# Optimization experiments

Measured on AMD Instinct MI355X. Metric: run time of the kernel, lower is better.

## Reference

```python
import jax, jax.numpy as jnp
import numpy as np

SPATIAL_SHAPES = [(128, 128), (64, 64), (32, 32), (16, 16)]  # (H_l, W_l) per level
NUM_HEADS = 8
NUM_LEVELS = 4
NUM_POINTS = 4
EMBED_DIM = 256
HEAD_DIM = EMBED_DIM // NUM_HEADS
LEN_V = sum(h * w for h, w in SPATIAL_SHAPES)  # 21760
BS, LQ = 8, 900


def setup_inputs() -> dict:
    key = jax.random.key(0)
    ks = jax.random.split(key, 12)
    s = 0.05
    return {
        'query': jax.random.normal(ks[0], (BS, LQ, EMBED_DIM), jnp.float32),
        'reference_points': jax.random.uniform(ks[1], (BS, LQ, NUM_LEVELS, 2), jnp.float32),
        'value': jax.random.normal(ks[2], (BS, LEN_V, EMBED_DIM), jnp.float32),
        'w_value': jax.random.normal(ks[3], (EMBED_DIM, EMBED_DIM), jnp.float32) * s,
        'b_value': jnp.zeros((EMBED_DIM,), jnp.float32),
        'w_off': jax.random.normal(ks[4], (EMBED_DIM, NUM_HEADS * NUM_LEVELS * NUM_POINTS * 2), jnp.float32) * s,
        'b_off': jax.random.normal(ks[5], (NUM_HEADS * NUM_LEVELS * NUM_POINTS * 2,), jnp.float32),
        'w_attn': jax.random.normal(ks[6], (EMBED_DIM, NUM_HEADS * NUM_LEVELS * NUM_POINTS), jnp.float32) * s,
        'b_attn': jnp.zeros((NUM_HEADS * NUM_LEVELS * NUM_POINTS,), jnp.float32),
        'w_out': jax.random.normal(ks[7], (EMBED_DIM, EMBED_DIM), jnp.float32) * s,
        'b_out': jnp.zeros((EMBED_DIM,), jnp.float32),
    }


def _bilinear_sample(val, locx, locy, H, W):
    # val: [bs, nh, H*W, hd]; locx/locy: [bs, nh, N] normalized in [0,1]
    # grid_sample semantics: align_corners=False, zero padding.
    px = locx * W - 0.5
    py = locy * H - 0.5
    x0 = jnp.floor(px)
    y0 = jnp.floor(py)
    dx = px - x0
    dy = py - y0
    x0i = x0.astype(jnp.int32)
    y0i = y0.astype(jnp.int32)
    out = jnp.zeros(val.shape[:2] + (locx.shape[-1], val.shape[-1]), val.dtype)
    corners = [
        (x0i, y0i, (1 - dx) * (1 - dy)),
        (x0i + 1, y0i, dx * (1 - dy)),
        (x0i, y0i + 1, (1 - dx) * dy),
        (x0i + 1, y0i + 1, dx * dy),
    ]
    for xi, yi, w in corners:
        valid = ((xi >= 0) & (xi < W) & (yi >= 0) & (yi < H)).astype(val.dtype)
        idx = jnp.clip(yi, 0, H - 1) * W + jnp.clip(xi, 0, W - 1)
        g = jnp.take_along_axis(val, idx[..., None], axis=2)  # [bs,nh,N,hd]
        out = out + g * (w * valid)[..., None]
    return out


def reference(query, reference_points, value, w_value, b_value, w_off, b_off,
              w_attn, b_attn, w_out, b_out):
    bs, Lq, C = query.shape
    # value projection -> [bs, Lv, nh, hd]
    v = (value @ w_value + b_value).reshape(bs, -1, NUM_HEADS, HEAD_DIM)
    # sampling offsets [bs,Lq,nh,L,P,2], attention weights softmax over L*P
    off = (query @ w_off + b_off).reshape(bs, Lq, NUM_HEADS, NUM_LEVELS, NUM_POINTS, 2)
    aw = (query @ w_attn + b_attn).reshape(bs, Lq, NUM_HEADS, NUM_LEVELS * NUM_POINTS)
    aw = jax.nn.softmax(aw, axis=-1).reshape(bs, Lq, NUM_HEADS, NUM_LEVELS, NUM_POINTS)
    # normalizer is (W_l, H_l) per level (flip of spatial shapes)
    norm = jnp.asarray([[w, h] for h, w in SPATIAL_SHAPES], query.dtype)  # [L,2]
    loc = reference_points[:, :, None, :, None, :] + off / norm[None, None, None, :, None, :]
    # per-level bilinear sampling and weighted reduction
    out = jnp.zeros((bs, Lq, NUM_HEADS, HEAD_DIM), query.dtype)
    start = 0
    for l, (H, W) in enumerate(SPATIAL_SHAPES):
        vl = v[:, start:start + H * W]                       # [bs,HW,nh,hd]
        vl = vl.transpose(0, 2, 1, 3)                        # [bs,nh,HW,hd]
        ll = loc[:, :, :, l].transpose(0, 2, 1, 3, 4)        # [bs,nh,Lq,P,2]
        ll = ll.reshape(bs, NUM_HEADS, Lq * NUM_POINTS, 2)
        s = _bilinear_sample(vl, ll[..., 0], ll[..., 1], H, W)
        s = s.reshape(bs, NUM_HEADS, Lq, NUM_POINTS, HEAD_DIM)
        out = out + jnp.einsum('bhqpd,bqhp->bqhd', s, aw[:, :, :, l])
        start += H * W
    out = out.reshape(bs, Lq, C)
    return out @ w_out + b_out
```

## Files before the change

kernel.cpp:

```cpp
#include <hip/hip_runtime.h>

#define BS 8
#define LQ 900
#define NH 8
#define NL 4
#define NP 4
#define HD 32
#define ED 256
#define LEN_V 21760

typedef __attribute__((ext_vector_type(8))) short bf16x8;
typedef __attribute__((ext_vector_type(4))) float f32x4;
typedef __attribute__((ext_vector_type(4))) float fv4;

static __device__ __forceinline__ unsigned short f2bf(float f) {
  union { float f; unsigned u; } x; x.f = f;
  unsigned r = x.u + 0x7fffu + ((x.u >> 16) & 1u);
  return (unsigned short)(r >> 16);
}
static __device__ __forceinline__ float bf2f(unsigned short s) {
  union { unsigned u; float f; } x; x.u = ((unsigned)s) << 16;
  return x.f;
}
static __device__ __forceinline__ unsigned pack2(float a, float b) {
  return (unsigned)f2bf(a) | ((unsigned)f2bf(b) << 16);
}

__global__ __launch_bounds__(256, 3) void vproj_kernel(
    const float* __restrict__ value, const float* __restrict__ w,
    const float* __restrict__ bias, unsigned short* __restrict__ vout) {
  const int t = threadIdx.x;
  const int row0 = blockIdx.x * 64;
  const int wv = t >> 6;
  const int lane = t & 63;
  const int quad = lane >> 4;
  const int nn = lane & 15;

  __shared__ unsigned short a_lds[4 * 64 * 8];
  __shared__ unsigned short b_lds[4 * 256 * 8];

  f32x4 acc[4][4];
#pragma unroll
  for (int i = 0; i < 4; i++)
#pragma unroll
    for (int j = 0; j < 4; j++) acc[i][j] = (f32x4)(0.f);

  const int arow = t >> 2;
  const int akseg = t & 3;
  const int bkseg = wv;
  const int bn = lane;

  for (int k0 = 0; k0 < 256; k0 += 32) {
    __syncthreads();
    {
      const float* pa = &value[(row0 + arow) * 256 + k0 + akseg * 8];
      fv4 v0 = __builtin_nontemporal_load((const fv4*)pa);
      fv4 v1 = __builtin_nontemporal_load((const fv4*)(pa + 4));
      uint4 pk;
      pk.x = pack2(v0.x, v0.y);
      pk.y = pack2(v0.z, v0.w);
      pk.z = pack2(v1.x, v1.y);
      pk.w = pack2(v1.z, v1.w);
      *(uint4*)&a_lds[(akseg * 64 + arow) * 8] = pk;
    }
    {
      const float* pb = &w[(k0 + bkseg * 8) * 256 + bn];
#pragma unroll
      for (int c = 0; c < 4; c++) {
        float f[8];
#pragma unroll
        for (int j = 0; j < 8; j++) f[j] = pb[j * 256 + c * 64];
        uint4 pk;
        pk.x = pack2(f[0], f[1]);
        pk.y = pack2(f[2], f[3]);
        pk.z = pack2(f[4], f[5]);
        pk.w = pack2(f[6], f[7]);
        *(uint4*)&b_lds[(bkseg * 256 + c * 64 + bn) * 8] = pk;
      }
    }
    __syncthreads();

    bf16x8 af[4], bf[4];
#pragma unroll
    for (int rt = 0; rt < 4; rt++)
      af[rt] = *(const bf16x8*)&a_lds[(quad * 64 + rt * 16 + nn) * 8];
#pragma unroll
    for (int ct = 0; ct < 4; ct++)
      bf[ct] = *(const bf16x8*)&b_lds[(quad * 256 + wv * 64 + ct * 16 + nn) * 8];
#pragma unroll
    for (int rt = 0; rt < 4; rt++)
#pragma unroll
      for (int ct = 0; ct < 4; ct++)
        acc[rt][ct] = __builtin_amdgcn_mfma_f32_16x16x32_bf16(
            af[rt], bf[ct], acc[rt][ct], 0, 0, 0);
  }

#pragma unroll
  for (int ct = 0; ct < 4; ct++) {
    const int col = wv * 64 + ct * 16 + nn;
    const float bv = bias[col];
    const int h = col >> 5;
    const int d = col & 31;
#pragma unroll
    for (int rt = 0; rt < 4; rt++) {
      f32x4 f = acc[rt][ct];
#pragma unroll
      for (int reg = 0; reg < 4; reg++) {
        const int grow = row0 + rt * 16 + quad * 4 + reg;
        const int b = grow / LEN_V;
        const int s = grow - b * LEN_V;
        vout[((b * NH + h) * LEN_V + s) * HD + d] = f2bf(f[reg] + bv);
      }
    }
  }
}

__global__ __launch_bounds__(256, 4) void msda_kernel(
    const float* __restrict__ query, const float* __restrict__ refp,
    const unsigned short* __restrict__ vp,
    const float* __restrict__ w_off, const float* __restrict__ b_off,
    const float* __restrict__ w_attn, const float* __restrict__ b_attn,
    const float* __restrict__ w_out, const float* __restrict__ b_out,
    float* __restrict__ out) {
  const int t = threadIdx.x;
  const int b = blockIdx.x / (LQ / 4);
  const int q0 = (blockIdx.x % (LQ / 4)) * 4;

  __shared__ float q_lds[4][256];
  __shared__ float off_lds[4][256];
  __shared__ float aw_lds[4][128];
  __shared__ float res_lds[4][256];
  __shared__ float ref_lds[4][4][2];

#pragma unroll
  for (int qi = 0; qi < 4; qi++)
    q_lds[qi][t] = query[(b * LQ + q0 + qi) * 256 + t];
  if (t < 32) {
    const int qi = t >> 3, l = (t >> 1) & 3, xy = t & 1;
    ref_lds[qi][l][xy] = refp[((b * LQ + q0 + qi) * NL + l) * 2 + xy];
  }
  __syncthreads();

  {
    const float bo = b_off[t];
    float acc[4];
#pragma unroll
    for (int qi = 0; qi < 4; qi++) acc[qi] = bo;
    for (int c = 0; c < 256; c += 4) {
      const float w0 = w_off[(c + 0) * 256 + t];
      const float w1 = w_off[(c + 1) * 256 + t];
      const float w2 = w_off[(c + 2) * 256 + t];
      const float w3 = w_off[(c + 3) * 256 + t];
#pragma unroll
      for (int qi = 0; qi < 4; qi++) {
        const float4 qv = *(const float4*)&q_lds[qi][c];
        acc[qi] += qv.x * w0 + qv.y * w1 + qv.z * w2 + qv.w * w3;
      }
    }
#pragma unroll
    for (int qi = 0; qi < 4; qi++) off_lds[qi][t] = acc[qi];
  }

  {
    const int col = t & 127;
    const int qb = (t >> 7) * 2;
    const float ba = b_attn[col];
    float acc0 = ba, acc1 = ba;
    for (int c = 0; c < 256; c += 4) {
      const float w0 = w_attn[(c + 0) * 128 + col];
      const float w1 = w_attn[(c + 1) * 128 + col];
      const float w2 = w_attn[(c + 2) * 128 + col];
      const float w3 = w_attn[(c + 3) * 128 + col];
      const float4 qv0 = *(const float4*)&q_lds[qb][c];
      const float4 qv1 = *(const float4*)&q_lds[qb + 1][c];
      acc0 += qv0.x * w0 + qv0.y * w1 + qv0.z * w2 + qv0.w * w3;
      acc1 += qv1.x * w0 + qv1.y * w1 + qv1.z * w2 + qv1.w * w3;
    }
    aw_lds[qb][col] = acc0;
    aw_lds[qb + 1][col] = acc1;
  }
  __syncthreads();

  if (t < 32) {
    const int qi = t >> 3, h = t & 7;
    float* a = &aw_lds[qi][h * 16];
    float m = a[0];
#pragma unroll
    for (int i = 1; i < 16; i++) m = fmaxf(m, a[i]);
    float e[16];
    float ssum = 0.f;
#pragma unroll
    for (int i = 0; i < 16; i++) { e[i] = __expf(a[i] - m); ssum += e[i]; }
    const float inv = 1.f / ssum;
#pragma unroll
    for (int i = 0; i < 16; i++) a[i] = e[i] * inv;
  }
  __syncthreads();

  const int h = t >> 5;
  const int d = t & 31;
  const int lvlW[4] = {128, 64, 32, 16};
  const int lvlH[4] = {128, 64, 32, 16};
  const int lvlS[4] = {0, 16384, 20480, 21504};
  const int vbase = (b * NH + h) * LEN_V * HD;
  float racc[4] = {0.f, 0.f, 0.f, 0.f};
#pragma unroll
  for (int l = 0; l < 4; l++) {
    const int W = lvlW[l], H = lvlH[l];
    const float Wf = (float)W, Hf = (float)H;
    const unsigned short* vl = vp + vbase + lvlS[l] * HD + d;
#pragma unroll
    for (int qi = 0; qi < 4; qi++) {
      const float refx = ref_lds[qi][l][0];
      const float refy = ref_lds[qi][l][1];
#pragma unroll
      for (int p = 0; p < 4; p++) {
        const float offx = off_lds[qi][h * 32 + l * 8 + p * 2 + 0];
        const float offy = off_lds[qi][h * 32 + l * 8 + p * 2 + 1];
        const float aw = aw_lds[qi][h * 16 + l * 4 + p];
        const float px = refx * Wf + offx - 0.5f;
        const float py = refy * Hf + offy - 0.5f;
        const float x0f = floorf(px), y0f = floorf(py);
        const float dx = px - x0f, dy = py - y0f;
        const int x0 = (int)x0f, y0 = (int)y0f;
        const int x1 = x0 + 1, y1 = y0 + 1;
        const float mx0 = (x0 >= 0 && x0 < W) ? 1.f : 0.f;
        const float mx1 = (x1 >= 0 && x1 < W) ? 1.f : 0.f;
        const float my0 = (y0 >= 0 && y0 < H) ? 1.f : 0.f;
        const float my1 = (y1 >= 0 && y1 < H) ? 1.f : 0.f;
        const int x0c = min(max(x0, 0), W - 1);
        const int x1c = min(max(x1, 0), W - 1);
        const int y0c = min(max(y0, 0), H - 1);
        const int y1c = min(max(y1, 0), H - 1);
        const float w00 = (1.f - dx) * (1.f - dy) * mx0 * my0;
        const float w10 = dx * (1.f - dy) * mx1 * my0;
        const float w01 = (1.f - dx) * dy * mx0 * my1;
        const float w11 = dx * dy * mx1 * my1;
        const float v00 = bf2f(vl[(y0c * W + x0c) * HD]);
        const float v10 = bf2f(vl[(y0c * W + x1c) * HD]);
        const float v01 = bf2f(vl[(y1c * W + x0c) * HD]);
        const float v11 = bf2f(vl[(y1c * W + x1c) * HD]);
        racc[qi] += aw * (w00 * v00 + w10 * v10 + w01 * v01 + w11 * v11);
      }
    }
  }
#pragma unroll
  for (int qi = 0; qi < 4; qi++) res_lds[qi][h * HD + d] = racc[qi];
  __syncthreads();

  {
    const float bo = b_out[t];
    float acc[4];
#pragma unroll
    for (int qi = 0; qi < 4; qi++) acc[qi] = bo;
    for (int c = 0; c < 256; c += 4) {
      const float w0 = w_out[(c + 0) * 256 + t];
      const float w1 = w_out[(c + 1) * 256 + t];
      const float w2 = w_out[(c + 2) * 256 + t];
      const float w3 = w_out[(c + 3) * 256 + t];
#pragma unroll
      for (int qi = 0; qi < 4; qi++) {
        const float4 rv = *(const float4*)&res_lds[qi][c];
        acc[qi] += rv.x * w0 + rv.y * w1 + rv.z * w2 + rv.w * w3;
      }
    }
#pragma unroll
    for (int qi = 0; qi < 4; qi++)
      out[(b * LQ + q0 + qi) * 256 + t] = acc[qi];
  }
}

extern "C" void kernel_launch(void* const* d_in, const int* in_sizes, int n_in,
                              void* d_out, int out_size, void* d_ws, size_t ws_size,
                              hipStream_t stream) {
  (void)in_sizes; (void)n_in; (void)out_size; (void)ws_size;
  const float* query   = (const float*)d_in[0];
  const float* refp    = (const float*)d_in[1];
  const float* value   = (const float*)d_in[2];
  const float* w_value = (const float*)d_in[3];
  const float* b_value = (const float*)d_in[4];
  const float* w_off   = (const float*)d_in[5];
  const float* b_off   = (const float*)d_in[6];
  const float* w_attn  = (const float*)d_in[7];
  const float* b_attn  = (const float*)d_in[8];
  const float* w_out   = (const float*)d_in[9];
  const float* b_out   = (const float*)d_in[10];
  float* out = (float*)d_out;
  unsigned short* vp = (unsigned short*)d_ws;

  vproj_kernel<<<(BS * LEN_V) / 64, 256, 0, stream>>>(value, w_value, b_value, vp);
  msda_kernel<<<BS * (LQ / 4), 256, 0, stream>>>(query, refp, vp, w_off, b_off,
                                                 w_attn, b_attn, w_out, b_out, out);
}
```

Measured before the change: 435.1 us.

## Split fused MSDA kernel into tiled projection, sampling, and output-projection kernels

Splits the monolithic per-4-query kernel into three kernels. A register-tiled GEMM computes offsets and attention logits for 32 rows at a time. A sampling kernel precomputes corner offsets and combined weights into LDS and gathers two bf16 channels per 32-bit load. A separate tiled GEMM does the output projection. The aim is more weight reuse in the small GEMMs, which before reread weights from global memory for every 4 queries, plus a leaner gather loop. The cost is extra kernel launches and round trips through global memory for the intermediates.

```diff
diff --git a/kernel.cpp b/kernel.cpp
--- a/kernel.cpp
+++ b/kernel.cpp
@@ -115,69 +115,88 @@
   }
 }
 
-__global__ __launch_bounds__(256, 4) void msda_kernel(
-    const float* __restrict__ query, const float* __restrict__ refp,
-    const unsigned short* __restrict__ vp,
+__global__ __launch_bounds__(384, 2) void offattn_kernel(
+    const float* __restrict__ query,
     const float* __restrict__ w_off, const float* __restrict__ b_off,
     const float* __restrict__ w_attn, const float* __restrict__ b_attn,
-    const float* __restrict__ w_out, const float* __restrict__ b_out,
-    float* __restrict__ out) {
+    float* __restrict__ OFF, float* __restrict__ LOG) {
+  const int t = threadIdx.x;
+  const int row0 = blockIdx.x * 32;
+  const int rg = t / 96;
+  const int c4 = t % 96;
+  const int col = c4 * 4;
+  const bool isOff = col < 256;
+  const float* wbase = isOff ? (w_off + col) : (w_attn + (col - 256));
+  const int wstride = isOff ? 256 : 128;
+  const float* bb = isOff ? (b_off + col) : (b_attn + (col - 256));
+  __shared__ float a_lds[32][8];
+
+  float4 acc[8];
+#pragma unroll
+  for (int r = 0; r < 8; r++) acc[r] = make_float4(0.f, 0.f, 0.f, 0.f);
+
+  for (int k0 = 0; k0 < 256; k0 += 8) {
+    __syncthreads();
+    if (t < 256) a_lds[t >> 3][t & 7] = query[(row0 + (t >> 3)) * 256 + k0 + (t & 7)];
+    __syncthreads();
+    float4 wr[8];
+#pragma unroll
+    for (int k = 0; k < 8; k++)
+      wr[k] = *(const float4*)&wbase[(k0 + k) * wstride];
+#pragma unroll
+    for (int r = 0; r < 8; r++) {
+      const float* ar = &a_lds[rg * 8 + r][0];
+      float4 a0 = *(const float4*)&ar[0];
+      float4 a1 = *(const float4*)&ar[4];
+      float4 s = acc[r];
+      s.x += a0.x*wr[0].x + a0.y*wr[1].x + a0.z*wr[2].x + a0.w*wr[3].x
+           + a1.x*wr[4].x + a1.y*wr[5].x + a1.z*wr[6].x + a1.w*wr[7].x;
+      s.y += a0.x*wr[0].y + a0.y*wr[1].y + a0.z*wr[2].y + a0.w*wr[3].y
+           + a1.x*wr[4].y + a1.y*wr[5].y + a1.z*wr[6].y + a1.w*wr[7].y;
+      s.z += a0.x*wr[0].z + a0.y*wr[1].z + a0.z*wr[2].z + a0.w*wr[3].z
+           + a1.x*wr[4].z + a1.y*wr[5].z + a1.z*wr[6].z + a1.w*wr[7].z;
+      s.w += a0.x*wr[0].w + a0.y*wr[1].w + a0.z*wr[2].w + a0.w*wr[3].w
+           + a1.x*wr[4].w + a1.y*wr[5].w + a1.z*wr[6].w + a1.w*wr[7].w;
+      acc[r] = s;
+    }
+  }
+
+  const float4 bv = *(const float4*)bb;
+#pragma unroll
+  for (int r = 0; r < 8; r++) {
+    const int grow = row0 + rg * 8 + r;
+    float4 o = make_float4(acc[r].x + bv.x, acc[r].y + bv.y,
+                           acc[r].z + bv.z, acc[r].w + bv.w);
+    if (isOff) *(float4*)&OFF[grow * 256 + col] = o;
+    else       *(float4*)&LOG[grow * 128 + (col - 256)] = o;
+  }
+}
+
+__global__ __launch_bounds__(256, 4) void sample_kernel(
+    const float* __restrict__ refp, const unsigned short* __restrict__ vp,
+    const float* __restrict__ OFF, const float* __restrict__ LOG,
+    float* __restrict__ RES) {
   const int t = threadIdx.x;
   const int b = blockIdx.x / (LQ / 4);
   const int q0 = (blockIdx.x % (LQ / 4)) * 4;
 
-  __shared__ float q_lds[4][256];
   __shared__ float off_lds[4][256];
   __shared__ float aw_lds[4][128];
-  __shared__ float res_lds[4][256];
   __shared__ float ref_lds[4][4][2];
+  __shared__ int   soff[512][4];
+  __shared__ float swt[512][4];
 
 #pragma unroll
   for (int qi = 0; qi < 4; qi++)
-    q_lds[qi][t] = query[(b * LQ + q0 + qi) * 256 + t];
+    off_lds[qi][t] = OFF[(b * LQ + q0 + qi) * 256 + t];
+  if (t < 128) {
+#pragma unroll
+    for (int qi = 0; qi < 4; qi++)
+      aw_lds[qi][t] = LOG[(b * LQ + q0 + qi) * 128 + t];
+  }
   if (t < 32) {
     const int qi = t >> 3, l = (t >> 1) & 3, xy = t & 1;
     ref_lds[qi][l][xy] = refp[((b * LQ + q0 + qi) * NL + l) * 2 + xy];
-  }
-  __syncthreads();
-
-  {
-    const float bo = b_off[t];
-    float acc[4];
-#pragma unroll
-    for (int qi = 0; qi < 4; qi++) acc[qi] = bo;
-    for (int c = 0; c < 256; c += 4) {
-      const float w0 = w_off[(c + 0) * 256 + t];
-      const float w1 = w_off[(c + 1) * 256 + t];
-      const float w2 = w_off[(c + 2) * 256 + t];
-      const float w3 = w_off[(c + 3) * 256 + t];
-#pragma unroll
-      for (int qi = 0; qi < 4; qi++) {
-        const float4 qv = *(const float4*)&q_lds[qi][c];
-        acc[qi] += qv.x * w0 + qv.y * w1 + qv.z * w2 + qv.w * w3;
-      }
-    }
-#pragma unroll
-    for (int qi = 0; qi < 4; qi++) off_lds[qi][t] = acc[qi];
-  }
-
-  {
-    const int col = t & 127;
-    const int qb = (t >> 7) * 2;
-    const float ba = b_attn[col];
-    float acc0 = ba, acc1 = ba;
-    for (int c = 0; c < 256; c += 4) {
-      const float w0 = w_attn[(c + 0) * 128 + col];
-      const float w1 = w_attn[(c + 1) * 128 + col];
-      const float w2 = w_attn[(c + 2) * 128 + col];
-      const float w3 = w_attn[(c + 3) * 128 + col];
-      const float4 qv0 = *(const float4*)&q_lds[qb][c];
-      const float4 qv1 = *(const float4*)&q_lds[qb + 1][c];
-      acc0 += qv0.x * w0 + qv0.y * w1 + qv0.z * w2 + qv0.w * w3;
-      acc1 += qv1.x * w0 + qv1.y * w1 + qv1.z * w2 + qv1.w * w3;
-    }
-    aw_lds[qb][col] = acc0;
-    aw_lds[qb + 1][col] = acc1;
   }
   __syncthreads();
 
@@ -197,76 +216,122 @@
   }
   __syncthreads();
 
-  const int h = t >> 5;
-  const int d = t & 31;
-  const int lvlW[4] = {128, 64, 32, 16};
-  const int lvlH[4] = {128, 64, 32, 16};
-  const int lvlS[4] = {0, 16384, 20480, 21504};
-  const int vbase = (b * NH + h) * LEN_V * HD;
-  float racc[4] = {0.f, 0.f, 0.f, 0.f};
-#pragma unroll
-  for (int l = 0; l < 4; l++) {
-    const int W = lvlW[l], H = lvlH[l];
-    const float Wf = (float)W, Hf = (float)H;
-    const unsigned short* vl = vp + vbase + lvlS[l] * HD + d;
-#pragma unroll
-    for (int qi = 0; qi < 4; qi++) {
-      const float refx = ref_lds[qi][l][0];
-      const float refy = ref_lds[qi][l][1];
-#pragma unroll
-      for (int p = 0; p < 4; p++) {
-        const float offx = off_lds[qi][h * 32 + l * 8 + p * 2 + 0];
-        const float offy = off_lds[qi][h * 32 + l * 8 + p * 2 + 1];
-        const float aw = aw_lds[qi][h * 16 + l * 4 + p];
-        const float px = refx * Wf + offx - 0.5f;
-        const float py = refy * Hf + offy - 0.5f;
-        const float x0f = floorf(px), y0f = floorf(py);
-        const float dx = px - x0f, dy = py - y0f;
-        const int x0 = (int)x0f, y0 = (int)y0f;
-        const int x1 = x0 + 1, y1 = y0 + 1;
-        const float mx0 = (x0 >= 0 && x0 < W) ? 1.f : 0.f;
-        const float mx1 = (x1 >= 0 && x1 < W) ? 1.f : 0.f;
-        const float my0 = (y0 >= 0 && y0 < H) ? 1.f : 0.f;
-        const float my1 = (y1 >= 0 && y1 < H) ? 1.f : 0.f;
-        const int x0c = min(max(x0, 0), W - 1);
-        const int x1c = min(max(x1, 0), W - 1);
-        const int y0c = min(max(y0, 0), H - 1);
-        const int y1c = min(max(y1, 0), H - 1);
-        const float w00 = (1.f - dx) * (1.f - dy) * mx0 * my0;
-        const float w10 = dx * (1.f - dy) * mx1 * my0;
-        const float w01 = (1.f - dx) * dy * mx0 * my1;
-        const float w11 = dx * dy * mx1 * my1;
-        const float v00 = bf2f(vl[(y0c * W + x0c) * HD]);
-        const float v10 = bf2f(vl[(y0c * W + x1c) * HD]);
-        const float v01 = bf2f(vl[(y1c * W + x0c) * HD]);
-        const float v11 = bf2f(vl[(y1c * W + x1c) * HD]);
-        racc[qi] += aw * (w00 * v00 + w10 * v10 + w01 * v01 + w11 * v11);
-      }
-    }
-  }
-#pragma unroll
-  for (int qi = 0; qi < 4; qi++) res_lds[qi][h * HD + d] = racc[qi];
+#pragma unroll
+  for (int ss = 0; ss < 2; ss++) {
+    const int sid = t + ss * 256;
+    const int p = sid & 3, l = (sid >> 2) & 3, h = (sid >> 4) & 7, qi = sid >> 7;
+    const int W = 128 >> l;
+    const int base = (l == 0) ? 0 : ((l == 1) ? 16384 : ((l == 2) ? 20480 : 21504));
+    const float Wf = (float)W;
+    const float refx = ref_lds[qi][l][0];
+    const float refy = ref_lds[qi][l][1];
+    const float offx = off_lds[qi][h * 32 + l * 8 + p * 2 + 0];
+    const float offy = off_lds[qi][h * 32 + l * 8 + p * 2 + 1];
+    const float aw = aw_lds[qi][h * 16 + l * 4 + p];
+    const float px = refx * Wf + offx - 0.5f;
+    const float py = refy * Wf + offy - 0.5f;
+    const float x0f = floorf(px), y0f = floorf(py);
+    const float dx = px - x0f, dy = py - y0f;
+    const int x0 = (int)x0f, y0 = (int)y0f;
+    const int x1 = x0 + 1, y1 = y0 + 1;
+    const float mx0 = (x0 >= 0 && x0 < W) ? 1.f : 0.f;
+    const float mx1 = (x1 >= 0 && x1 < W) ? 1.f : 0.f;
+    const float my0 = (y0 >= 0 && y0 < W) ? 1.f : 0.f;
+    const float my1 = (y1 >= 0 && y1 < W) ? 1.f : 0.f;
+    const int x0c = min(max(x0, 0), W - 1);
+    const int x1c = min(max(x1, 0), W - 1);
+    const int y0c = min(max(y0, 0), W - 1);
+    const int y1c = min(max(y1, 0), W - 1);
+    soff[sid][0] = (base + y0c * W + x0c) * 16;
+    soff[sid][1] = (base + y0c * W + x1c) * 16;
+    soff[sid][2] = (base + y1c * W + x0c) * 16;
+    soff[sid][3] = (base + y1c * W + x1c) * 16;
+    swt[sid][0] = (1.f - dx) * (1.f - dy) * mx0 * my0 * aw;
+    swt[sid][1] = dx * (1.f - dy) * mx1 * my0 * aw;
+    swt[sid][2] = (1.f - dx) * dy * mx0 * my1 * aw;
+    swt[sid][3] = dx * dy * mx1 * my1 * aw;
+  }
   __syncthreads();
 
-  {
-    const float bo = b_out[t];
-    float acc[4];
-#pragma unroll
-    for (int qi = 0; qi < 4; qi++) acc[qi] = bo;
-    for (int c = 0; c < 256; c += 4) {
-      const float w0 = w_out[(c + 0) * 256 + t];
-      const float w1 = w_out[(c + 1) * 256 + t];
-      const float w2 = w_out[(c + 2) * 256 + t];
-      const float w3 = w_out[(c + 3) * 256 + t];
-#pragma unroll
-      for (int qi = 0; qi < 4; qi++) {
-        const float4 rv = *(const float4*)&res_lds[qi][c];
-        acc[qi] += rv.x * w0 + rv.y * w1 + rv.z * w2 + rv.w * w3;
-      }
-    }
-#pragma unroll
-    for (int qi = 0; qi < 4; qi++)
-      out[(b * LQ + q0 + qi) * 256 + t] = acc[qi];
+  const int qsel = t >> 7;
+  const int hh = (t >> 4) & 7;
+  const int d2 = t & 15;
+  const unsigned* vpu = (const unsigned*)vp + (size_t)(b * NH + hh) * (LEN_V * HD / 2);
+#pragma unroll
+  for (int j = 0; j < 2; j++) {
+    const int qi = qsel * 2 + j;
+    float r0 = 0.f, r1 = 0.f;
+#pragma unroll
+    for (int lp = 0; lp < 16; lp++) {
+      const int sid = ((qi * 8 + hh) << 4) + lp;
+      const int4 o = *(const int4*)&soff[sid][0];
+      const float4 w = *(const float4*)&swt[sid][0];
+      const unsigned u00 = vpu[o.x + d2];
+      const unsigned u10 = vpu[o.y + d2];
+      const unsigned u01 = vpu[o.z + d2];
+      const unsigned u11 = vpu[o.w + d2];
+      r0 += w.x * bf2f((unsigned short)(u00 & 0xffff))
+          + w.y * bf2f((unsigned short)(u10 & 0xffff))
+          + w.z * bf2f((unsigned short)(u01 & 0xffff))
+          + w.w * bf2f((unsigned short)(u11 & 0xffff));
+      r1 += w.x * bf2f((unsigned short)(u00 >> 16))
+          + w.y * bf2f((unsigned short)(u10 >> 16))
+          + w.z * bf2f((unsigned short)(u01 >> 16))
+          + w.w * bf2f((unsigned short)(u11 >> 16));
+    }
+    float2 rr = make_float2(r0, r1);
+    *(float2*)&RES[(b * LQ + q0 + qi) * 256 + hh * 32 + d2 * 2] = rr;
+  }
+}
+
+__global__ __launch_bounds__(256, 2) void outproj_kernel(
+    const float* __restrict__ RES, const float* __restrict__ w,
+    const float* __restrict__ bias, float* __restrict__ out) {
+  const int t = threadIdx.x;
+  const int row0 = blockIdx.x * 32;
+  const int rg = t >> 6;
+  const int c0 = (t & 63) << 2;
+  __shared__ float a_lds[32][8];
+
+  float4 acc[8];
+#pragma unroll
+  for (int r = 0; r < 8; r++) acc[r] = make_float4(0.f, 0.f, 0.f, 0.f);
+
+  const int lr = t >> 3;
+  const int lk = t & 7;
+  for (int k0 = 0; k0 < 256; k0 += 8) {
+    __syncthreads();
+    a_lds[lr][lk] = RES[(row0 + lr) * 256 + k0 + lk];
+    __syncthreads();
+    float4 wr[8];
+#pragma unroll
+    for (int k = 0; k < 8; k++)
+      wr[k] = *(const float4*)&w[(k0 + k) * 256 + c0];
+#pragma unroll
+    for (int r = 0; r < 8; r++) {
+      const float* ar = &a_lds[rg * 8 + r][0];
+      float4 a0 = *(const float4*)&ar[0];
+      float4 a1 = *(const float4*)&ar[4];
+      float4 s = acc[r];
+      s.x += a0.x*wr[0].x + a0.y*wr[1].x + a0.z*wr[2].x + a0.w*wr[3].x
+           + a1.x*wr[4].x + a1.y*wr[5].x + a1.z*wr[6].x + a1.w*wr[7].x;
+      s.y += a0.x*wr[0].y + a0.y*wr[1].y + a0.z*wr[2].y + a0.w*wr[3].y
+           + a1.x*wr[4].y + a1.y*wr[5].y + a1.z*wr[6].y + a1.w*wr[7].y;
+      s.z += a0.x*wr[0].z + a0.y*wr[1].z + a0.z*wr[2].z + a0.w*wr[3].z
+           + a1.x*wr[4].z + a1.y*wr[5].z + a1.z*wr[6].z + a1.w*wr[7].z;
+      s.w += a0.x*wr[0].w + a0.y*wr[1].w + a0.z*wr[2].w + a0.w*wr[3].w
+           + a1.x*wr[4].w + a1.y*wr[5].w + a1.z*wr[6].w + a1.w*wr[7].w;
+      acc[r] = s;
+    }
+  }
+
+  const float4 bv = *(const float4*)&bias[c0];
+#pragma unroll
+  for (int r = 0; r < 8; r++) {
+    const int grow = row0 + rg * 8 + r;
+    float4 o = make_float4(acc[r].x + bv.x, acc[r].y + bv.y,
+                           acc[r].z + bv.z, acc[r].w + bv.w);
+    *(float4*)&out[grow * 256 + c0] = o;
   }
 }
 
@@ -286,9 +351,16 @@
   const float* w_out   = (const float*)d_in[9];
   const float* b_out   = (const float*)d_in[10];
   float* out = (float*)d_out;
-  unsigned short* vp = (unsigned short*)d_ws;
+
+  char* ws = (char*)d_ws;
+  unsigned short* vp = (unsigned short*)ws;
+  float* OFF = (float*)(ws + 89128960);
+  float* LOG = (float*)(ws + 89128960 + 7372800);
+  float* RES = (float*)(ws + 89128960 + 7372800 + 3686400);
 
   vproj_kernel<<<(BS * LEN_V) / 64, 256, 0, stream>>>(value, w_value, b_value, vp);
-  msda_kernel<<<BS * (LQ / 4), 256, 0, stream>>>(query, refp, vp, w_off, b_off,
-                                                 w_attn, b_attn, w_out, b_out, out);
-}
+  offattn_kernel<<<(BS * LQ) / 32, 384, 0, stream>>>(query, w_off, b_off,
+                                                     w_attn, b_attn, OFF, LOG);
+  sample_kernel<<<BS * (LQ / 4), 256, 0, stream>>>(refp, vp, OFF, LOG, RES);
+  outproj_kernel<<<(BS * LQ) / 32, 256, 0, stream>>>(RES, w_out, b_out, out);
+}
```

Result: no change. 443.1 us (+1.8%).
